# Performance work log

Hardware: AMD Instinct MI355X
Metric: run time of the kernel (lower is better)

## Reference

```python
import jax, jax.numpy as jnp
import numpy as np

PS = 8  # patch_size


def setup_inputs() -> dict:
    key = jax.random.key(0)
    k1, k2 = jax.random.split(key)
    shape = (16, 3, 512, 512)
    return {
        "input": jax.random.normal(k1, shape, dtype=jnp.float32),
        "target": jax.random.normal(k2, shape, dtype=jnp.float32),
    }


def _extract_patches(x):
    # (B,C,H,W) -> (B,C,nh,nw,ps,ps); H,W assumed divisible by PS (no pad needed)
    B, C, H, W = x.shape
    x = x.reshape(B, C, H // PS, PS, W // PS, PS)
    return jnp.transpose(x, (0, 1, 2, 4, 3, 5))


def _fft_feats(patches):
    fft = jnp.fft.fft2(patches, norm="ortho")          # over last two axes
    fft = jnp.fft.fftshift(fft, axes=(-2, -1))
    real, imag = fft.real, fft.imag
    # log1p norm: sign(x) * log1p(|x|)
    real = jnp.sign(real) * jnp.log1p(jnp.abs(real))
    imag = jnp.sign(imag) * jnp.log1p(jnp.abs(imag))
    return real, imag


def reference(input, target):
    ir, ii = _fft_feats(_extract_patches(input))
    tr, ti = _fft_feats(_extract_patches(target))
    loss = (ir - tr) ** 2 + (ii - ti) ** 2   # mse real + mse imag, unreduced
    return jnp.mean(loss)
```

## Files before the change

### kernel.cpp

```cpp
#include <hip/hip_runtime.h>

#define SQ1_2 0.70710678118654752440f

__device__ __forceinline__ float g_feat(float x) {
    return copysignf(__logf(1.0f + fabsf(x)), x);
}

__device__ __forceinline__ void rfft8(const float r[8], float o[8]) {
    float s0 = r[0] + r[4], d0 = r[0] - r[4];
    float s1 = r[1] + r[5], d1 = r[1] - r[5];
    float s2 = r[2] + r[6], d2 = r[2] - r[6];
    float s3 = r[3] + r[7], d3 = r[3] - r[7];
    float ss02 = s0 + s2, sd02 = s0 - s2;
    float ss13 = s1 + s3, sd13 = s1 - s3;
    float t1 = SQ1_2 * (d1 - d3);
    float t2 = SQ1_2 * (d1 + d3);
    o[0] = ss02 + ss13;
    o[1] = ss02 - ss13;
    o[2] = d0 + t1;
    o[3] = -(d2 + t2);
    o[4] = sd02;
    o[5] = -sd13;
    o[6] = d0 - t1;
    o[7] = d2 - t2;
}

__device__ __forceinline__ void cfft8(const float xr[8], const float xi[8],
                                      float Fr[8], float Fi[8]) {
    float s0r = xr[0] + xr[4], s0i = xi[0] + xi[4], d0r = xr[0] - xr[4], d0i = xi[0] - xi[4];
    float s1r = xr[1] + xr[5], s1i = xi[1] + xi[5], d1r = xr[1] - xr[5], d1i = xi[1] - xi[5];
    float s2r = xr[2] + xr[6], s2i = xi[2] + xi[6], d2r = xr[2] - xr[6], d2i = xi[2] - xi[6];
    float s3r = xr[3] + xr[7], s3i = xi[3] + xi[7], d3r = xr[3] - xr[7], d3i = xi[3] - xi[7];
    float ss0r = s0r + s2r, ss0i = s0i + s2i, sd0r = s0r - s2r, sd0i = s0i - s2i;
    float ss1r = s1r + s3r, ss1i = s1i + s3i, sd1r = s1r - s3r, sd1i = s1i - s3i;
    Fr[0] = ss0r + ss1r; Fi[0] = ss0i + ss1i;
    Fr[4] = ss0r - ss1r; Fi[4] = ss0i - ss1i;
    Fr[2] = sd0r + sd1i; Fi[2] = sd0i - sd1r;
    Fr[6] = sd0r - sd1i; Fi[6] = sd0i + sd1r;
    float t1r = SQ1_2 * (d1r + d1i), t1i = SQ1_2 * (d1i - d1r);
    float t2r = d2i,                 t2i = -d2r;
    float t3r = SQ1_2 * (d3i - d3r), t3i = -SQ1_2 * (d3r + d3i);
    float ts0r = d0r + t2r, ts0i = d0i + t2i, td0r = d0r - t2r, td0i = d0i - t2i;
    float ts1r = t1r + t3r, ts1i = t1i + t3i, td1r = t1r - t3r, td1i = t1i - t3i;
    Fr[1] = ts0r + ts1r; Fi[1] = ts0i + ts1i;
    Fr[5] = ts0r - ts1r; Fi[5] = ts0i - ts1i;
    Fr[3] = td0r + td1i; Fi[3] = td0i - td1r;
    Fr[7] = td0r - td1i; Fi[7] = td0i + td1r;
}

__global__ __launch_bounds__(256, 5) void patchfft_loss_kernel(
        const float* __restrict__ in, const float* __restrict__ tgt,
        float* __restrict__ out) {
    int t = blockIdx.x * 256 + threadIdx.x;
    int lane = t & 63;
    int w = t >> 6;
    int pi = w * 32 + (lane & 31);
    const float* src = (lane >= 32) ? tgt : in;

    int pw = pi & 63;
    int ph = (pi >> 6) & 63;
    int bc = pi >> 12;
    long base = (long)bc * 262144 + ph * 4096 + pw * 8;

    float v[64];
    #pragma unroll
    for (int m = 0; m < 8; ++m) {
        const float4* p4 = reinterpret_cast<const float4*>(src + base + (long)m * 512);
        float4 a0 = p4[0];
        float4 a1 = p4[1];
        float r[8] = {a0.x * 0.125f, a0.y * 0.125f, a0.z * 0.125f, a0.w * 0.125f,
                      a1.x * 0.125f, a1.y * 0.125f, a1.z * 0.125f, a1.w * 0.125f};
        rfft8(r, &v[m * 8]);
    }

    float acc1 = 0.0f, acc2 = 0.0f;
    #pragma unroll
    for (int j = 0; j < 2; ++j) {
        float c[8], o[8];
        #pragma unroll
        for (int m = 0; m < 8; ++m) c[m] = v[m * 8 + j];
        rfft8(c, o);
        #pragma unroll
        for (int k = 0; k < 8; ++k) {
            float fm = g_feat(o[k]);
            float d = fm - __shfl_xor(fm, 32, 64);
            if (k < 2) acc1 += d * d;
            else       acc2 += d * d;
        }
    }
    #pragma unroll
    for (int l = 0; l < 3; ++l) {
        float cr[8], ci[8], Fr[8], Fi[8];
        #pragma unroll
        for (int m = 0; m < 8; ++m) {
            cr[m] = v[m * 8 + 2 + 2 * l];
            ci[m] = v[m * 8 + 3 + 2 * l];
        }
        cfft8(cr, ci, Fr, Fi);
        #pragma unroll
        for (int k = 0; k < 8; ++k) {
            float fr = g_feat(Fr[k]);
            float fi = g_feat(Fi[k]);
            float dr = fr - __shfl_xor(fr, 32, 64);
            float di = fi - __shfl_xor(fi, 32, 64);
            acc2 += dr * dr + di * di;
        }
    }
    float loss = acc1 + 2.0f * acc2;

    #pragma unroll
    for (int off = 32; off > 0; off >>= 1) loss += __shfl_down(loss, off, 64);
    __shared__ float wsum[4];
    int wid = threadIdx.x >> 6;
    if ((threadIdx.x & 63) == 0) wsum[wid] = loss;
    __syncthreads();
    if (threadIdx.x == 0) {
        float s = wsum[0] + wsum[1] + wsum[2] + wsum[3];
        atomicAdd(out, s * (1.0f / 25165824.0f));
    }
}

extern "C" void kernel_launch(void* const* d_in, const int* in_sizes, int n_in,
                              void* d_out, int out_size, void* d_ws, size_t ws_size,
                              hipStream_t stream) {
    const float* in  = (const float*)d_in[0];
    const float* tgt = (const float*)d_in[1];
    float* out = (float*)d_out;
    (void)in_sizes; (void)n_in; (void)d_ws; (void)ws_size; (void)out_size;

    hipMemsetAsync(out, 0, sizeof(float), stream);
    patchfft_loss_kernel<<<1536, 256, 0, stream>>>(in, tgt, out);
}
```

Before: 124.2 us.

## Split per-patch FFT across threads via LDS and pack real columns into complex FFT

Each patch is now handled by four threads instead of one. They do the row FFTs, exchange results through swizzled shared memory, and then each runs one complex column FFT. The two purely real columns are packed into a single complex FFT and separated afterwards using conjugate symmetry. The single global atomic is replaced by 256 spread partial sums plus a small final reduction kernel. The aim is to cut register pressure (64 floats per thread), raise occupancy and reduce atomic contention, at the cost of LDS traffic, a barrier and an extra launch.

```diff
diff --git a/kernel.cpp b/kernel.cpp
--- a/kernel.cpp
+++ b/kernel.cpp
@@ -48,76 +48,111 @@
     Fr[7] = td0r - td1i; Fi[7] = td0i + td1r;
 }
 
-__global__ __launch_bounds__(256, 5) void patchfft_loss_kernel(
+__global__ __launch_bounds__(256, 8) void patchfft_stage_kernel(
         const float* __restrict__ in, const float* __restrict__ tgt,
-        float* __restrict__ out) {
-    int t = blockIdx.x * 256 + threadIdx.x;
-    int lane = t & 63;
-    int w = t >> 6;
-    int pi = w * 32 + (lane & 31);
-    const float* src = (lane >= 32) ? tgt : in;
+        float* __restrict__ partial) {
+    __shared__ float lds[4096];
+    __shared__ float wsum[4];
+    const int tid = threadIdx.x;
 
-    int pw = pi & 63;
-    int ph = (pi >> 6) & 63;
-    int bc = pi >> 12;
-    long base = (long)bc * 262144 + ph * 4096 + pw * 8;
-
-    float v[64];
-    #pragma unroll
-    for (int m = 0; m < 8; ++m) {
-        const float4* p4 = reinterpret_cast<const float4*>(src + base + (long)m * 512);
-        float4 a0 = p4[0];
-        float4 a1 = p4[1];
-        float r[8] = {a0.x * 0.125f, a0.y * 0.125f, a0.z * 0.125f, a0.w * 0.125f,
-                      a1.x * 0.125f, a1.y * 0.125f, a1.z * 0.125f, a1.w * 0.125f};
-        rfft8(r, &v[m * 8]);
-    }
-
-    float acc1 = 0.0f, acc2 = 0.0f;
-    #pragma unroll
-    for (int j = 0; j < 2; ++j) {
-        float c[8], o[8];
+    {
+        const int pair = tid >> 3;
+        const int T    = (tid >> 2) & 1;
+        const int r2   = tid & 3;
+        const int p  = blockIdx.x * 32 + pair;
+        const int pw = p & 63;
+        const int ph = (p >> 6) & 63;
+        const int bc = p >> 12;
+        const long base = (long)bc * 262144 + ph * 4096 + pw * 8;
+        const float* __restrict__ src = T ? tgt : in;
+        const int tp = pair * 2 + T;
+        const int s  = tp & 7;
         #pragma unroll
-        for (int m = 0; m < 8; ++m) c[m] = v[m * 8 + j];
-        rfft8(c, o);
-        #pragma unroll
-        for (int k = 0; k < 8; ++k) {
-            float fm = g_feat(o[k]);
-            float d = fm - __shfl_xor(fm, 32, 64);
-            if (k < 2) acc1 += d * d;
-            else       acc2 += d * d;
+        for (int mm = 0; mm < 2; ++mm) {
+            const int m = 2 * r2 + mm;
+            const float4* p4 = reinterpret_cast<const float4*>(src + base + (long)m * 512);
+            float4 a0 = p4[0];
+            float4 a1 = p4[1];
+            float r[8] = {a0.x * 0.125f, a0.y * 0.125f, a0.z * 0.125f, a0.w * 0.125f,
+                          a1.x * 0.125f, a1.y * 0.125f, a1.z * 0.125f, a1.w * 0.125f};
+            float o[8];
+            rfft8(r, o);
+            float4* dst = reinterpret_cast<float4*>(&lds[tp * 64 + ((m ^ s) << 3)]);
+            dst[0] = make_float4(o[0], o[1], o[2], o[3]);
+            dst[1] = make_float4(o[4], o[5], o[6], o[7]);
         }
     }
-    #pragma unroll
-    for (int l = 0; l < 3; ++l) {
-        float cr[8], ci[8], Fr[8], Fi[8];
+    __syncthreads();
+
+    float loss;
+    {
+        const int pair = tid >> 3;
+        const int T    = (tid >> 2) & 1;
+        const int task = tid & 3;
+        const int tp = pair * 2 + T;
+        const int s  = tp & 7;
+        float zr[8], zi[8];
         #pragma unroll
         for (int m = 0; m < 8; ++m) {
-            cr[m] = v[m * 8 + 2 + 2 * l];
-            ci[m] = v[m * 8 + 3 + 2 * l];
+            float2 z = *reinterpret_cast<const float2*>(
+                &lds[tp * 64 + ((m ^ s) << 3) + task * 2]);
+            zr[m] = z.x;
+            zi[m] = z.y;
         }
-        cfft8(cr, ci, Fr, Fi);
-        #pragma unroll
-        for (int k = 0; k < 8; ++k) {
-            float fr = g_feat(Fr[k]);
-            float fi = g_feat(Fi[k]);
-            float dr = fr - __shfl_xor(fr, 32, 64);
-            float di = fi - __shfl_xor(fi, 32, 64);
-            acc2 += dr * dr + di * di;
+        float Fr[8], Fi[8];
+        cfft8(zr, zi, Fr, Fi);
+
+        float acc1 = 0.0f, acc2 = 0.0f;
+        if (task == 0) {
+            float w0 = g_feat(Fr[0]), w1 = g_feat(Fr[4]);
+            float w2 = g_feat(Fi[0]), w3 = g_feat(Fi[4]);
+            float d0 = w0 - __shfl_xor(w0, 4, 64);
+            float d1 = w1 - __shfl_xor(w1, 4, 64);
+            float d2 = w2 - __shfl_xor(w2, 4, 64);
+            float d3 = w3 - __shfl_xor(w3, 4, 64);
+            acc1 = d0 * d0 + d1 * d1 + d2 * d2 + d3 * d3;
+            #pragma unroll
+            for (int k = 1; k <= 3; ++k) {
+                float v0 = 0.5f * (Fr[k] + Fr[8 - k]);
+                float v1 = 0.5f * (Fi[k] - Fi[8 - k]);
+                float v2 = 0.5f * (Fi[k] + Fi[8 - k]);
+                float v3 = 0.5f * (Fr[k] - Fr[8 - k]);
+                float f0 = g_feat(v0), f1 = g_feat(v1), f2 = g_feat(v2), f3 = g_feat(v3);
+                float e0 = f0 - __shfl_xor(f0, 4, 64);
+                float e1 = f1 - __shfl_xor(f1, 4, 64);
+                float e2 = f2 - __shfl_xor(f2, 4, 64);
+                float e3 = f3 - __shfl_xor(f3, 4, 64);
+                acc2 += e0 * e0 + e1 * e1 + e2 * e2 + e3 * e3;
+            }
+        } else {
+            #pragma unroll
+            for (int k = 0; k < 8; ++k) {
+                float fr = g_feat(Fr[k]);
+                float fi = g_feat(Fi[k]);
+                float dr = fr - __shfl_xor(fr, 4, 64);
+                float di = fi - __shfl_xor(fi, 4, 64);
+                acc2 += dr * dr + di * di;
+            }
         }
+        loss = acc1 + 2.0f * acc2;
     }
-    float loss = acc1 + 2.0f * acc2;
 
     #pragma unroll
     for (int off = 32; off > 0; off >>= 1) loss += __shfl_down(loss, off, 64);
-    __shared__ float wsum[4];
-    int wid = threadIdx.x >> 6;
-    if ((threadIdx.x & 63) == 0) wsum[wid] = loss;
+    if ((tid & 63) == 0) wsum[tid >> 6] = loss;
     __syncthreads();
-    if (threadIdx.x == 0) {
-        float s = wsum[0] + wsum[1] + wsum[2] + wsum[3];
-        atomicAdd(out, s * (1.0f / 25165824.0f));
+    if (tid == 0) {
+        atomicAdd(&partial[blockIdx.x & 255], wsum[0] + wsum[1] + wsum[2] + wsum[3]);
     }
+}
+
+__global__ void patchfft_final_kernel(const float* __restrict__ partial,
+                                      float* __restrict__ out) {
+    float s = partial[threadIdx.x] + partial[threadIdx.x + 64]
+            + partial[threadIdx.x + 128] + partial[threadIdx.x + 192];
+    #pragma unroll
+    for (int off = 32; off > 0; off >>= 1) s += __shfl_down(s, off, 64);
+    if (threadIdx.x == 0) *out = s * (1.0f / 25165824.0f);
 }
 
 extern "C" void kernel_launch(void* const* d_in, const int* in_sizes, int n_in,
@@ -126,8 +161,10 @@
     const float* in  = (const float*)d_in[0];
     const float* tgt = (const float*)d_in[1];
     float* out = (float*)d_out;
-    (void)in_sizes; (void)n_in; (void)d_ws; (void)ws_size; (void)out_size;
+    float* partial = (float*)d_ws;
+    (void)in_sizes; (void)n_in; (void)ws_size; (void)out_size;
 
-    hipMemsetAsync(out, 0, sizeof(float), stream);
-    patchfft_loss_kernel<<<1536, 256, 0, stream>>>(in, tgt, out);
+    hipMemsetAsync(partial, 0, 256 * sizeof(float), stream);
+    patchfft_stage_kernel<<<6144, 256, 0, stream>>>(in, tgt, partial);
+    patchfft_final_kernel<<<1, 64, 0, stream>>>(partial, out);
 }
```

Result: no change. 124.4 us (+0.2%).

## Stage patch rows through LDS with direct global-to-LDS loads and two-level reduction

Applied to the files above, without the earlier changes.

Each 64-thread block now loads 32 patches from both tensors with global_load_lds, so a wavefront reads contiguous 1 KB rows coalesced instead of strided 32-byte chunks per thread. Threads then read their 8x8 patch from LDS. The single atomic to the output is replaced by atomics spread over 256 partial slots in the workspace, followed by a small final reduction kernel. This adds an extra kernel launch and a memset, and uses 16 KB of LDS per 64-thread block, which may limit occupancy.

```diff
diff --git a/kernel.cpp b/kernel.cpp
--- a/kernel.cpp
+++ b/kernel.cpp
@@ -1,4 +1,5 @@
 #include <hip/hip_runtime.h>
+#include <stdint.h>
 
 #define SQ1_2 0.70710678118654752440f
 
@@ -48,28 +49,42 @@
     Fr[7] = td0r - td1i; Fi[7] = td0i + td1r;
 }
 
-__global__ __launch_bounds__(256, 5) void patchfft_loss_kernel(
+__global__ __launch_bounds__(64) void patchfft_stage_kernel(
         const float* __restrict__ in, const float* __restrict__ tgt,
-        float* __restrict__ out) {
-    int t = blockIdx.x * 256 + threadIdx.x;
-    int lane = t & 63;
-    int w = t >> 6;
-    int pi = w * 32 + (lane & 31);
-    const float* src = (lane >= 32) ? tgt : in;
+        float* __restrict__ partial) {
+    __shared__ float lds[4096];
+    const int lane = threadIdx.x;
 
-    int pw = pi & 63;
-    int ph = (pi >> 6) & 63;
-    int bc = pi >> 12;
-    long base = (long)bc * 262144 + ph * 4096 + pw * 8;
+    const int p0 = blockIdx.x * 32;
+    const int pw0 = p0 & 63;
+    const int ph  = (p0 >> 6) & 63;
+    const int bc  = p0 >> 12;
+    const long gbase = (long)bc * 262144 + (long)ph * 4096 + pw0 * 8;
+
+    #pragma unroll
+    for (int c = 0; c < 16; ++c) {
+        const int T = c >> 3;
+        const int m = c & 7;
+        const float* src = T ? tgt : in;
+        const float* gp = src + gbase + (long)m * 512 + lane * 4;
+        __builtin_amdgcn_global_load_lds(
+            (const __attribute__((address_space(1))) void*)gp,
+            (__attribute__((address_space(3))) void*)&lds[c * 256],
+            16, 0, 0);
+    }
+    __syncthreads();
+
+    const int Ts = lane >> 5;
+    const int q  = lane & 31;
 
     float v[64];
     #pragma unroll
     for (int m = 0; m < 8; ++m) {
-        const float4* p4 = reinterpret_cast<const float4*>(src + base + (long)m * 512);
-        float4 a0 = p4[0];
-        float4 a1 = p4[1];
-        float r[8] = {a0.x * 0.125f, a0.y * 0.125f, a0.z * 0.125f, a0.w * 0.125f,
-                      a1.x * 0.125f, a1.y * 0.125f, a1.z * 0.125f, a1.w * 0.125f};
+        const float4* row = reinterpret_cast<const float4*>(&lds[(Ts * 8 + m) * 256 + q * 8]);
+        float4 lo = row[0];
+        float4 hi = row[1];
+        float r[8] = {lo.x * 0.125f, lo.y * 0.125f, lo.z * 0.125f, lo.w * 0.125f,
+                      hi.x * 0.125f, hi.y * 0.125f, hi.z * 0.125f, hi.w * 0.125f};
         rfft8(r, &v[m * 8]);
     }
 
@@ -110,14 +125,18 @@
 
     #pragma unroll
     for (int off = 32; off > 0; off >>= 1) loss += __shfl_down(loss, off, 64);
-    __shared__ float wsum[4];
-    int wid = threadIdx.x >> 6;
-    if ((threadIdx.x & 63) == 0) wsum[wid] = loss;
-    __syncthreads();
-    if (threadIdx.x == 0) {
-        float s = wsum[0] + wsum[1] + wsum[2] + wsum[3];
-        atomicAdd(out, s * (1.0f / 25165824.0f));
+    if (lane == 0) {
+        atomicAdd(&partial[blockIdx.x & 255], loss);
     }
+}
+
+__global__ void patchfft_final_kernel(const float* __restrict__ partial,
+                                      float* __restrict__ out) {
+    float s = partial[threadIdx.x] + partial[threadIdx.x + 64]
+            + partial[threadIdx.x + 128] + partial[threadIdx.x + 192];
+    #pragma unroll
+    for (int off = 32; off > 0; off >>= 1) s += __shfl_down(s, off, 64);
+    if (threadIdx.x == 0) *out = s * (1.0f / 25165824.0f);
 }
 
 extern "C" void kernel_launch(void* const* d_in, const int* in_sizes, int n_in,
@@ -126,8 +145,10 @@
     const float* in  = (const float*)d_in[0];
     const float* tgt = (const float*)d_in[1];
     float* out = (float*)d_out;
-    (void)in_sizes; (void)n_in; (void)d_ws; (void)ws_size; (void)out_size;
+    float* partial = (float*)d_ws;
+    (void)in_sizes; (void)n_in; (void)ws_size; (void)out_size;
 
-    hipMemsetAsync(out, 0, sizeof(float), stream);
-    patchfft_loss_kernel<<<1536, 256, 0, stream>>>(in, tgt, out);
+    hipMemsetAsync(partial, 0, 256 * sizeof(float), stream);
+    patchfft_stage_kernel<<<6144, 64, 0, stream>>>(in, tgt, partial);
+    patchfft_final_kernel<<<1, 64, 0, stream>>>(partial, out);
 }
```

Measured after the change: 123.4 us. No clear change (-0.6%).
